# Kernel optimization log

Hardware: AMD Instinct MI355X
Metric: run time of the kernel (lower is better)

## Reference

```python
import jax, jax.numpy as jnp
import numpy as np

L = 8  # uniform FSQ levels per channel (same for every channel)
COMMIT = 0.25


def setup_inputs() -> dict:
    key = jax.random.key(0)
    ks = jax.random.split(key, 8)
    B, S, D, K = 16, 4096, 512, 256
    return {
        "x": jax.random.normal(ks[0], (B, S, D), jnp.float32),
        "codebook": jax.random.normal(ks[1], (K, D), jnp.float32),
        "channel_means": jax.random.normal(ks[2], (D,), jnp.float32) * 0.1,
        "channel_stds": jax.random.uniform(ks[3], (D,), jnp.float32, 0.75, 1.25),
        "w1": jax.random.normal(ks[4], (D, D // 2), jnp.float32) * 0.02,
        "b1": jnp.zeros((D // 2,), jnp.float32),
        "w2": jax.random.normal(ks[5], (D // 2, 2), jnp.float32) * 0.02,
        "b2": jnp.zeros((2,), jnp.float32),
    }


def _uniform_fsq(x):
    # argmin over linspace(-1,1,L) == round to nearest grid point after clamping
    step = 2.0 / (L - 1)
    xc = jnp.clip(x, -1.0, 1.0)
    idx = jnp.round((xc + 1.0) / step)          # [B,S,D] float indices in [0,L-1]
    q = -1.0 + idx * step                        # gathered bound values
    q_st = x + jax.lax.stop_gradient(q - x)
    loss = COMMIT * jnp.mean((x - jax.lax.stop_gradient(q)) ** 2)
    return q_st, idx.astype(jnp.int32), loss


def _kmeans_fsq(x, codebook, means, stds):
    # eval-mode quantize: normalize, cdist+argmin (squared distances share argmin), gather, denorm
    xn = (x - means) / stds                                          # [B,S,D]
    x2 = jnp.sum(xn * xn, axis=-1, keepdims=True)                    # [B,S,1]
    c2 = jnp.sum(codebook * codebook, axis=-1)                       # [K]
    xc = jnp.einsum("bsd,kd->bsk", xn, codebook)                     # [B,S,K]
    d2 = x2 - 2.0 * xc + c2                                          # squared cdist
    indices = jnp.argmin(d2, axis=-1)                                # [B,S]
    q = codebook[indices] * stds + means                             # [B,S,D]
    q_st = x + jax.lax.stop_gradient(q - x)
    loss = COMMIT * jnp.mean((x - jax.lax.stop_gradient(q)) ** 2)
    return q_st, indices, loss


def reference(x, codebook, channel_means, channel_stds, w1, b1, w2, b2):
    # codebook selector on mean-pooled sequence (eval mode: plain softmax)
    pooled = jnp.mean(x, axis=1)                                     # [B,D]
    h = jax.nn.relu(pooled @ w1 + b1)
    logits = h @ w2 + b2                                             # [B,2]
    weights = jax.nn.softmax(logits, axis=-1)                        # [B,2]

    q_u, idx_u, loss_u = _uniform_fsq(x)
    q_k, idx_k, loss_k = _kmeans_fsq(x, codebook, channel_means, channel_stds)

    uw = weights[:, 0][:, None, None]
    kw = weights[:, 1][:, None, None]
    quantized = uw * q_u + kw * q_k                                  # [B,S,D]
    total_loss = loss_u + loss_k
    return quantized, total_loss, idx_k, weights
```

## Files before the change

kernel.cpp:

```cpp
#include <hip/hip_runtime.h>
#include <math.h>

typedef __bf16 bf16x8 __attribute__((ext_vector_type(8)));
typedef float f32x4 __attribute__((ext_vector_type(4)));
typedef unsigned short ushort_t;
typedef unsigned int uint_t;

#define BB 16
#define SS 4096
#define DDIM 512
#define NCODE 256
#define MTOK 65536

#define LOSS_OFF 33554432
#define IDX_OFF  33554433
#define WGT_OFF  33619969

#define WS_LOSS 0
#define WS_LOG  128
#define WS_WGT  192
#define WS_POOL 256
#define WS_C2   8448
#define WS_RSTD 8704
#define WS_BAR  9216

__device__ __forceinline__ void async16(void* lds, const void* gptr) {
  __builtin_amdgcn_global_load_lds(
      (const __attribute__((address_space(1))) unsigned int*)(gptr),
      (__attribute__((address_space(3))) unsigned int*)(lds),
      16, 0, 0);
}

__global__ void init_ws(const float* __restrict__ stds, float* ws) {
  int i = blockIdx.x * blockDim.x + threadIdx.x;
  if (i < 8704) ws[i] = 0.f;
  else if (i < 9216) ws[WS_RSTD + (i - 8704)] = 1.f / stds[i - 8704];
  else if (i == 9216) ws[i] = 0.f;
}

__global__ __launch_bounds__(64) void c2_convert(
    const float* __restrict__ cb, float* __restrict__ c2,
    bf16x8* __restrict__ cbt) {
  const int k = blockIdx.x, t = threadIdx.x;
  const float4* row = (const float4*)(cb + (size_t)k * DDIM);
  float4 a = row[t * 2], b = row[t * 2 + 1];
  float v[8] = {a.x, a.y, a.z, a.w, b.x, b.y, b.z, b.w};
  bf16x8 hi, lo;
  float s = 0.f;
  #pragma unroll
  for (int j = 0; j < 8; j++) {
    s = fmaf(v[j], v[j], s);
    __bf16 hh = (__bf16)v[j];
    hi[j] = hh;
    lo[j] = (__bf16)(v[j] - (float)hh);
  }
  const int kb = t >> 2, q = t & 3;
  const int slot = k * 4 + (q ^ ((k >> 1) & 3));
  cbt[kb * 1024 + slot] = hi;
  cbt[16384 + kb * 1024 + slot] = lo;
  for (int m = 1; m <= 32; m <<= 1) s += __shfl_xor(s, m, 64);
  if (t == 0) c2[k] = s;
}

__global__ __launch_bounds__(512) void pool_kernel(const float* __restrict__ x,
                                                   float* __restrict__ pool) {
  int b = blockIdx.x, sc = blockIdx.y, d = threadIdx.x;
  const float* p = x + ((size_t)b * SS + (size_t)sc * 256) * DDIM + d;
  float s = 0.f;
  #pragma unroll 8
  for (int i = 0; i < 256; i++) s += p[(size_t)i * DDIM];
  atomicAdd(&pool[b * DDIM + d], s);
}

__global__ __launch_bounds__(256) void selector(
    const float* __restrict__ poolsum, const float* __restrict__ w1,
    const float* __restrict__ b1, const float* __restrict__ w2,
    const float* __restrict__ b2, float* __restrict__ wgt,
    float* __restrict__ out) {
  const int b = blockIdx.x, t = threadIdx.x;
  __shared__ float pl[512];
  pl[t] = poolsum[b * DDIM + t] * (1.f / SS);
  pl[t + 256] = poolsum[b * DDIM + 256 + t] * (1.f / SS);
  __syncthreads();
  float acc = 0.f;
  #pragma unroll 8
  for (int d = 0; d < DDIM; d++) acc = fmaf(pl[d], w1[d * 256 + t], acc);
  float hv = fmaxf(acc + b1[t], 0.f);
  float p0 = hv * w2[t * 2], p1 = hv * w2[t * 2 + 1];
  #pragma unroll
  for (int m = 1; m <= 32; m <<= 1) {
    p0 += __shfl_xor(p0, m, 64);
    p1 += __shfl_xor(p1, m, 64);
  }
  __shared__ float r0[4], r1[4];
  const int w = t >> 6;
  if ((t & 63) == 0) { r0[w] = p0; r1[w] = p1; }
  __syncthreads();
  if (t == 0) {
    float l0 = r0[0] + r0[1] + r0[2] + r0[3] + b2[0];
    float l1 = r1[0] + r1[1] + r1[2] + r1[3] + b2[1];
    float mx = fmaxf(l0, l1);
    float e0 = expf(l0 - mx), e1 = expf(l1 - mx);
    float inv = 1.f / (e0 + e1);
    wgt[b * 2] = e0 * inv; wgt[b * 2 + 1] = e1 * inv;
    out[WGT_OFF + b * 2] = e0 * inv; out[WGT_OFF + b * 2 + 1] = e1 * inv;
  }
}

__device__ __forceinline__ void grid_barrier(uint_t* cnt, uint_t nb) {
  __syncthreads();
  if (threadIdx.x == 0) {
    __hip_atomic_fetch_add(cnt, 1u, __ATOMIC_ACQ_REL, __HIP_MEMORY_SCOPE_AGENT);
    while (__hip_atomic_load(cnt, __ATOMIC_ACQUIRE, __HIP_MEMORY_SCOPE_AGENT) < nb)
      __builtin_amdgcn_s_sleep(2);
  }
  __syncthreads();
}

__global__ __launch_bounds__(256, 2) void gemm_fused(
    const float* __restrict__ x, const ushort_t* __restrict__ cbt,
    const float* __restrict__ means, const float* __restrict__ stds,
    const float* __restrict__ rstd, const float* __restrict__ cbf,
    const float* __restrict__ c2g, const float* __restrict__ wsel,
    float* __restrict__ out, float* __restrict__ idxout,
    float* __restrict__ loss_acc, uint_t* __restrict__ bar) {
  __shared__ bf16x8 Ahi[512], Alo[512], Bhi[1024], Blo[1024];
  __shared__ uint_t stash[4][32];
  __shared__ float slu[4], slk[4];
  const int tid = threadIdx.x;
  const int lane = tid & 63, w = tid >> 6;
  const size_t token0 = (size_t)blockIdx.x * 128;
  const int c = lane & 15, quad = lane >> 4;

  f32x4 acc[2][16];
  #pragma unroll
  for (int tt = 0; tt < 2; tt++)
    #pragma unroll
    for (int ct = 0; ct < 16; ct++) {
      f32x4 z = {0.f, 0.f, 0.f, 0.f};
      acc[tt][ct] = z;
    }

  const int r = tid >> 1, h = tid & 1;
  const float* xrow = x + (token0 + r) * DDIM;

  for (int kbi = 0; kbi < 16; kbi++) {
    const int kb = kbi * 32;
    __syncthreads();
    #pragma unroll
    for (int i = 0; i < 4; i++) {
      const int slot = i * 256 + tid;
      async16((void*)&Bhi[slot], (const void*)(cbt + ((size_t)kbi * 1024 + slot) * 8));
      async16((void*)&Blo[slot], (const void*)(cbt + ((size_t)(16384 + kbi * 1024) + slot) * 8));
    }
    #pragma unroll
    for (int sub = 0; sub < 2; sub++) {
      const int q = h * 2 + sub;
      const int kk = kb + q * 8;
      float4 xa = *(const float4*)(xrow + kk);
      float4 xb = *(const float4*)(xrow + kk + 4);
      float4 ma = *(const float4*)(means + kk);
      float4 mb = *(const float4*)(means + kk + 4);
      float4 ra = *(const float4*)(rstd + kk);
      float4 rb = *(const float4*)(rstd + kk + 4);
      float xv[8] = {xa.x, xa.y, xa.z, xa.w, xb.x, xb.y, xb.z, xb.w};
      float mv[8] = {ma.x, ma.y, ma.z, ma.w, mb.x, mb.y, mb.z, mb.w};
      float rv[8] = {ra.x, ra.y, ra.z, ra.w, rb.x, rb.y, rb.z, rb.w};
      bf16x8 hi, lo;
      #pragma unroll
      for (int j = 0; j < 8; j++) {
        float xn = (xv[j] - mv[j]) * rv[j];
        __bf16 hh = (__bf16)xn;
        hi[j] = hh;
        lo[j] = (__bf16)(xn - (float)hh);
      }
      const int p = (q + (r >> 1)) & 3;
      Ahi[r * 4 + p] = hi;
      Alo[r * 4 + p] = lo;
    }
    __syncthreads();

    bf16x8 ahi[2], alo[2];
    #pragma unroll
    for (int tt = 0; tt < 2; tt++) {
      const int rr = w * 32 + tt * 16 + c;
      const int p = (quad + (rr >> 1)) & 3;
      ahi[tt] = Ahi[rr * 4 + p];
      alo[tt] = Alo[rr * 4 + p];
    }
    #pragma unroll
    for (int ct = 0; ct < 16; ct++) {
      const int cf = ct * 16 + c;
      const int slot = cf * 4 + (quad ^ ((cf >> 1) & 3));
      bf16x8 bhi = Bhi[slot];
      bf16x8 blo = Blo[slot];
      #pragma unroll
      for (int tt = 0; tt < 2; tt++) {
        acc[tt][ct] = __builtin_amdgcn_mfma_f32_16x16x32_bf16(ahi[tt], bhi, acc[tt][ct], 0, 0, 0);
        acc[tt][ct] = __builtin_amdgcn_mfma_f32_16x16x32_bf16(ahi[tt], blo, acc[tt][ct], 0, 0, 0);
        acc[tt][ct] = __builtin_amdgcn_mfma_f32_16x16x32_bf16(alo[tt], bhi, acc[tt][ct], 0, 0, 0);
      }
    }
  }

  float c2v[16];
  #pragma unroll
  for (int ct = 0; ct < 16; ct++) c2v[ct] = c2g[ct * 16 + c];

#define LESS(av, ai, bv, bi) ((av) < (bv) || ((av) == (bv) && (ai) < (bi)))
#define INS2(v, i)                                                            \
  if (LESS(v, i, tv1, ti1)) {                                                 \
    tv1 = (v); ti1 = (i);                                                     \
    if (LESS(tv1, ti1, tv0, ti0)) { float tf = tv0; int tj = ti0; tv0 = tv1; ti0 = ti1; tv1 = tf; ti1 = tj; } \
  }

  #pragma unroll
  for (int tt = 0; tt < 2; tt++) {
    #pragma unroll
    for (int reg = 0; reg < 4; reg++) {
      float tv0 = 3.4e38f, tv1 = 3.4e38f;
      int ti0 = 0, ti1 = 0;
      #pragma unroll
      for (int ct = 0; ct < 16; ct++) {
        float vv = fmaf(-2.f, acc[tt][ct][reg], c2v[ct]);
        int ii = ct * 16 + c;
        INS2(vv, ii);
      }
      #pragma unroll
      for (int m = 1; m <= 8; m <<= 1) {
        float ov0 = __shfl_xor(tv0, m, 64), ov1 = __shfl_xor(tv1, m, 64);
        int oi0 = __shfl_xor(ti0, m, 64), oi1 = __shfl_xor(ti1, m, 64);
        INS2(ov0, oi0); INS2(ov1, oi1);
      }
      if (c == 0)
        stash[w][tt * 16 + quad * 4 + reg] = (uint_t)ti0 | ((uint_t)ti1 << 16);
    }
  }
#undef INS2
#undef LESS

  grid_barrier(bar, (uint_t)gridDim.x);

  const int dA = lane * 4;
  const int dB = 256 + lane * 4;
  float4 mA = *(const float4*)(means + dA), mB = *(const float4*)(means + dB);
  float4 sA = *(const float4*)(stds + dA),  sB = *(const float4*)(stds + dB);
  float4 rA = *(const float4*)(rstd + dA),  rB = *(const float4*)(rstd + dB);
  const float step = (float)(2.0 / 7.0);
  const int b = (int)(token0 >> 12);
  const float w0 = wsel[b * 2], w1v = wsel[b * 2 + 1];
  float lu = 0.f, lk = 0.f;

  #pragma unroll 2
  for (int it = 0; it < 32; it++) {
    const size_t token = token0 + (size_t)w * 32 + it;
    const uint_t packed = stash[w][it];
    const int k0 = (int)(packed & 0xffffu), k1 = (int)(packed >> 16);
    const float* xr = x + token * DDIM;
    float4 xA = *(const float4*)(xr + dA);
    float4 xB = *(const float4*)(xr + dB);
    const float* c0 = cbf + (size_t)k0 * DDIM;
    const float* c1 = cbf + (size_t)k1 * DDIM;
    float4 cA0 = *(const float4*)(c0 + dA), cB0 = *(const float4*)(c0 + dB);
    float4 cA1 = *(const float4*)(c1 + dA), cB1 = *(const float4*)(c1 + dB);

    float xnA0 = (xA.x - mA.x) * rA.x, xnA1 = (xA.y - mA.y) * rA.y;
    float xnA2 = (xA.z - mA.z) * rA.z, xnA3 = (xA.w - mA.w) * rA.w;
    float xnB0 = (xB.x - mB.x) * rB.x, xnB1 = (xB.y - mB.y) * rB.y;
    float xnB2 = (xB.z - mB.z) * rB.z, xnB3 = (xB.w - mB.w) * rB.w;

    float d0 = xnA0 * cA0.x + xnA1 * cA0.y + xnA2 * cA0.z + xnA3 * cA0.w +
               xnB0 * cB0.x + xnB1 * cB0.y + xnB2 * cB0.z + xnB3 * cB0.w;
    float d1 = xnA0 * cA1.x + xnA1 * cA1.y + xnA2 * cA1.z + xnA3 * cA1.w +
               xnB0 * cB1.x + xnB1 * cB1.y + xnB2 * cB1.z + xnB3 * cB1.w;
    #pragma unroll
    for (int m = 1; m <= 32; m <<= 1) {
      d0 += __shfl_xor(d0, m, 64);
      d1 += __shfl_xor(d1, m, 64);
    }
    float s0 = fmaf(-2.f, d0, c2g[k0]);
    float s1 = fmaf(-2.f, d1, c2g[k1]);
    const bool take1 = (s1 < s0) || (s1 == s0 && k1 < k0);
    const int bk = take1 ? k1 : k0;
    if (lane == 0) idxout[token] = (float)bk;
    float4 cwA, cwB;
    cwA = take1 ? cA1 : cA0;
    cwB = take1 ? cB1 : cB0;

    float4 oA, oB;
#define DOE(xx, cw, mm, ss, dst)                                              \
    { float xc = fminf(fmaxf(xx, -1.f), 1.f);                                 \
      float fi = rintf(__fdiv_rn(xc + 1.f, step));                            \
      float qq = __fadd_rn(__fmul_rn(fi, step), -1.f);                        \
      float qk = __fadd_rn(__fmul_rn(cw, ss), mm);                            \
      float qu_ = xx + (qq - xx);                                             \
      float qks = xx + (qk - xx);                                             \
      dst = w0 * qu_ + w1v * qks;                                             \
      float du = xx - qq; lu = fmaf(du, du, lu);                              \
      float dk = xx - qk; lk = fmaf(dk, dk, lk); }
    DOE(xA.x, cwA.x, mA.x, sA.x, oA.x)
    DOE(xA.y, cwA.y, mA.y, sA.y, oA.y)
    DOE(xA.z, cwA.z, mA.z, sA.z, oA.z)
    DOE(xA.w, cwA.w, mA.w, sA.w, oA.w)
    DOE(xB.x, cwB.x, mB.x, sB.x, oB.x)
    DOE(xB.y, cwB.y, mB.y, sB.y, oB.y)
    DOE(xB.z, cwB.z, mB.z, sB.z, oB.z)
    DOE(xB.w, cwB.w, mB.w, sB.w, oB.w)
#undef DOE
    f32x4 voA = {oA.x, oA.y, oA.z, oA.w};
    f32x4 voB = {oB.x, oB.y, oB.z, oB.w};
    __builtin_nontemporal_store(voA, (f32x4*)(out + token * DDIM + dA));
    __builtin_nontemporal_store(voB, (f32x4*)(out + token * DDIM + dB));
  }

  for (int m = 1; m <= 32; m <<= 1) {
    lu += __shfl_xor(lu, m, 64);
    lk += __shfl_xor(lk, m, 64);
  }
  if (lane == 0) { slu[w] = lu; slk[w] = lk; }
  __syncthreads();
  if (tid == 0) {
    atomicAdd(loss_acc + 0, slu[0] + slu[1] + slu[2] + slu[3]);
    atomicAdd(loss_acc + 64, slk[0] + slk[1] + slk[2] + slk[3]);
  }
}

__global__ void finalize_kernel(const float* __restrict__ ls, float* __restrict__ out_loss) {
  const float invN = 1.f / ((float)MTOK * (float)DDIM);
  out_loss[0] = 0.25f * (ls[0] * invN) + 0.25f * (ls[64] * invN);
}

extern "C" void kernel_launch(void* const* d_in, const int* in_sizes, int n_in,
                              void* d_out, int out_size, void* d_ws, size_t ws_size,
                              hipStream_t stream) {
  const float* x     = (const float*)d_in[0];
  const float* cbf   = (const float*)d_in[1];
  const float* means = (const float*)d_in[2];
  const float* stds  = (const float*)d_in[3];
  const float* w1    = (const float*)d_in[4];
  const float* b1    = (const float*)d_in[5];
  const float* w2    = (const float*)d_in[6];
  const float* b2    = (const float*)d_in[7];
  float* out = (float*)d_out;
  float* ws  = (float*)d_ws;
  bf16x8* cbt = (bf16x8*)d_out;

  hipLaunchKernelGGL(init_ws, dim3(37), dim3(256), 0, stream, stds, ws);
  hipLaunchKernelGGL(c2_convert, dim3(NCODE), dim3(64), 0, stream, cbf, ws + WS_C2, cbt);
  hipLaunchKernelGGL(pool_kernel, dim3(BB, 16), dim3(512), 0, stream, x, ws + WS_POOL);
  hipLaunchKernelGGL(selector, dim3(BB), dim3(256), 0, stream,
                     ws + WS_POOL, w1, b1, w2, b2, ws + WS_WGT, out);
  hipLaunchKernelGGL(gemm_fused, dim3(MTOK / 128), dim3(256), 0, stream,
                     x, (const ushort_t*)d_out, means, stds, ws + WS_RSTD, cbf,
                     ws + WS_C2, ws + WS_WGT, out, out + IDX_OFF, ws + WS_LOSS,
                     (uint_t*)(ws + WS_BAR));
  hipLaunchKernelGGL(finalize_kernel, dim3(1), dim3(1), 0, stream,
                     ws + WS_LOSS, out + LOSS_OFF);
}
```

Baseline: 386.8 us.

## Fuse mean-pooling and selector MLP into the persistent GEMM kernel

```diff
diff --git a/kernel.cpp b/kernel.cpp
--- a/kernel.cpp
+++ b/kernel.cpp
@@ -23,6 +23,7 @@
 #define WS_C2   8448
 #define WS_RSTD 8704
 #define WS_BAR  9216
+#define WS_BAR2 9217
 
 __device__ __forceinline__ void async16(void* lds, const void* gptr) {
   __builtin_amdgcn_global_load_lds(
@@ -35,7 +36,7 @@
   int i = blockIdx.x * blockDim.x + threadIdx.x;
   if (i < 8704) ws[i] = 0.f;
   else if (i < 9216) ws[WS_RSTD + (i - 8704)] = 1.f / stds[i - 8704];
-  else if (i == 9216) ws[i] = 0.f;
+  else if (i <= 9217) ws[i] = 0.f;
 }
 
 __global__ __launch_bounds__(64) void c2_convert(
@@ -62,51 +63,6 @@
   if (t == 0) c2[k] = s;
 }
 
-__global__ __launch_bounds__(512) void pool_kernel(const float* __restrict__ x,
-                                                   float* __restrict__ pool) {
-  int b = blockIdx.x, sc = blockIdx.y, d = threadIdx.x;
-  const float* p = x + ((size_t)b * SS + (size_t)sc * 256) * DDIM + d;
-  float s = 0.f;
-  #pragma unroll 8
-  for (int i = 0; i < 256; i++) s += p[(size_t)i * DDIM];
-  atomicAdd(&pool[b * DDIM + d], s);
-}
-
-__global__ __launch_bounds__(256) void selector(
-    const float* __restrict__ poolsum, const float* __restrict__ w1,
-    const float* __restrict__ b1, const float* __restrict__ w2,
-    const float* __restrict__ b2, float* __restrict__ wgt,
-    float* __restrict__ out) {
-  const int b = blockIdx.x, t = threadIdx.x;
-  __shared__ float pl[512];
-  pl[t] = poolsum[b * DDIM + t] * (1.f / SS);
-  pl[t + 256] = poolsum[b * DDIM + 256 + t] * (1.f / SS);
-  __syncthreads();
-  float acc = 0.f;
-  #pragma unroll 8
-  for (int d = 0; d < DDIM; d++) acc = fmaf(pl[d], w1[d * 256 + t], acc);
-  float hv = fmaxf(acc + b1[t], 0.f);
-  float p0 = hv * w2[t * 2], p1 = hv * w2[t * 2 + 1];
-  #pragma unroll
-  for (int m = 1; m <= 32; m <<= 1) {
-    p0 += __shfl_xor(p0, m, 64);
-    p1 += __shfl_xor(p1, m, 64);
-  }
-  __shared__ float r0[4], r1[4];
-  const int w = t >> 6;
-  if ((t & 63) == 0) { r0[w] = p0; r1[w] = p1; }
-  __syncthreads();
-  if (t == 0) {
-    float l0 = r0[0] + r0[1] + r0[2] + r0[3] + b2[0];
-    float l1 = r1[0] + r1[1] + r1[2] + r1[3] + b2[1];
-    float mx = fmaxf(l0, l1);
-    float e0 = expf(l0 - mx), e1 = expf(l1 - mx);
-    float inv = 1.f / (e0 + e1);
-    wgt[b * 2] = e0 * inv; wgt[b * 2 + 1] = e1 * inv;
-    out[WGT_OFF + b * 2] = e0 * inv; out[WGT_OFF + b * 2 + 1] = e1 * inv;
-  }
-}
-
 __device__ __forceinline__ void grid_barrier(uint_t* cnt, uint_t nb) {
   __syncthreads();
   if (threadIdx.x == 0) {
@@ -121,15 +77,19 @@
     const float* __restrict__ x, const ushort_t* __restrict__ cbt,
     const float* __restrict__ means, const float* __restrict__ stds,
     const float* __restrict__ rstd, const float* __restrict__ cbf,
-    const float* __restrict__ c2g, const float* __restrict__ wsel,
-    float* __restrict__ out, float* __restrict__ idxout,
-    float* __restrict__ loss_acc, uint_t* __restrict__ bar) {
+    const float* __restrict__ c2g, const float* __restrict__ w1,
+    const float* __restrict__ b1, const float* __restrict__ w2,
+    const float* __restrict__ b2, float* __restrict__ pool,
+    float* __restrict__ wsel, float* __restrict__ out,
+    float* __restrict__ idxout, float* __restrict__ loss_acc,
+    uint_t* __restrict__ bar, uint_t* __restrict__ bar2) {
   __shared__ bf16x8 Ahi[512], Alo[512], Bhi[1024], Blo[1024];
   __shared__ uint_t stash[4][32];
   __shared__ float slu[4], slk[4];
   const int tid = threadIdx.x;
   const int lane = tid & 63, w = tid >> 6;
   const size_t token0 = (size_t)blockIdx.x * 128;
+  const int b = (int)(token0 >> 12);
   const int c = lane & 15, quad = lane >> 4;
 
   f32x4 acc[2][16];
@@ -203,6 +163,25 @@
     }
   }
 
+  {
+    const int ch4 = (tid & 127) * 4;
+    const int rh = tid >> 7;
+    const float* px = x + (token0 + (size_t)rh * 64) * DDIM + ch4;
+    f32x4 p0 = {0.f,0.f,0.f,0.f}, p1 = {0.f,0.f,0.f,0.f};
+    f32x4 p2 = {0.f,0.f,0.f,0.f}, p3 = {0.f,0.f,0.f,0.f};
+    for (int i = 0; i < 64; i += 4) {
+      p0 += *(const f32x4*)(px + (size_t)(i + 0) * DDIM);
+      p1 += *(const f32x4*)(px + (size_t)(i + 1) * DDIM);
+      p2 += *(const f32x4*)(px + (size_t)(i + 2) * DDIM);
+      p3 += *(const f32x4*)(px + (size_t)(i + 3) * DDIM);
+    }
+    f32x4 ps = (p0 + p1) + (p2 + p3);
+    atomicAdd(&pool[b * DDIM + ch4 + 0], ps[0]);
+    atomicAdd(&pool[b * DDIM + ch4 + 1], ps[1]);
+    atomicAdd(&pool[b * DDIM + ch4 + 2], ps[2]);
+    atomicAdd(&pool[b * DDIM + ch4 + 3], ps[3]);
+  }
+
   float c2v[16];
   #pragma unroll
   for (int ct = 0; ct < 16; ct++) c2v[ct] = c2g[ct * 16 + c];
@@ -241,17 +220,57 @@
 
   grid_barrier(bar, (uint_t)gridDim.x);
 
+  __shared__ float selbuf[512];
+  __shared__ float sr0[4], sr1[4];
+  if (blockIdx.x < 16) {
+    const int sb = blockIdx.x;
+    float v0 = __hip_atomic_load(&pool[sb * DDIM + tid], __ATOMIC_RELAXED, __HIP_MEMORY_SCOPE_AGENT);
+    float v1 = __hip_atomic_load(&pool[sb * DDIM + 256 + tid], __ATOMIC_RELAXED, __HIP_MEMORY_SCOPE_AGENT);
+    selbuf[tid] = v0 * (1.f / SS);
+    selbuf[tid + 256] = v1 * (1.f / SS);
+    __syncthreads();
+    float a = 0.f;
+    #pragma unroll 8
+    for (int d = 0; d < DDIM; d++) a = fmaf(selbuf[d], w1[d * 256 + tid], a);
+    float hv = fmaxf(a + b1[tid], 0.f);
+    float q0 = hv * w2[tid * 2], q1 = hv * w2[tid * 2 + 1];
+    #pragma unroll
+    for (int m = 1; m <= 32; m <<= 1) {
+      q0 += __shfl_xor(q0, m, 64);
+      q1 += __shfl_xor(q1, m, 64);
+    }
+    if ((tid & 63) == 0) { sr0[tid >> 6] = q0; sr1[tid >> 6] = q1; }
+    __syncthreads();
+    if (tid == 0) {
+      float l0 = sr0[0] + sr0[1] + sr0[2] + sr0[3] + b2[0];
+      float l1 = sr1[0] + sr1[1] + sr1[2] + sr1[3] + b2[1];
+      float mx = fmaxf(l0, l1);
+      float e0 = expf(l0 - mx), e1 = expf(l1 - mx);
+      float inv = 1.f / (e0 + e1);
+      __hip_atomic_store(&wsel[sb * 2], e0 * inv, __ATOMIC_RELAXED, __HIP_MEMORY_SCOPE_AGENT);
+      __hip_atomic_store(&wsel[sb * 2 + 1], e1 * inv, __ATOMIC_RELAXED, __HIP_MEMORY_SCOPE_AGENT);
+      out[WGT_OFF + sb * 2] = e0 * inv;
+      out[WGT_OFF + sb * 2 + 1] = e1 * inv;
+      __hip_atomic_fetch_add(bar2, 1u, __ATOMIC_RELEASE, __HIP_MEMORY_SCOPE_AGENT);
+    }
+  }
+  if (tid == 0) {
+    while (__hip_atomic_load(bar2, __ATOMIC_ACQUIRE, __HIP_MEMORY_SCOPE_AGENT) < 16u)
+      __builtin_amdgcn_s_sleep(2);
+  }
+  __syncthreads();
+
   const int dA = lane * 4;
   const int dB = 256 + lane * 4;
   float4 mA = *(const float4*)(means + dA), mB = *(const float4*)(means + dB);
   float4 sA = *(const float4*)(stds + dA),  sB = *(const float4*)(stds + dB);
   float4 rA = *(const float4*)(rstd + dA),  rB = *(const float4*)(rstd + dB);
   const float step = (float)(2.0 / 7.0);
-  const int b = (int)(token0 >> 12);
-  const float w0 = wsel[b * 2], w1v = wsel[b * 2 + 1];
+  const float w0 = __hip_atomic_load(&wsel[b * 2], __ATOMIC_RELAXED, __HIP_MEMORY_SCOPE_AGENT);
+  const float w1v = __hip_atomic_load(&wsel[b * 2 + 1], __ATOMIC_RELAXED, __HIP_MEMORY_SCOPE_AGENT);
   float lu = 0.f, lk = 0.f;
 
-  #pragma unroll 2
+  #pragma unroll 4
   for (int it = 0; it < 32; it++) {
     const size_t token = token0 + (size_t)w * 32 + it;
     const uint_t packed = stash[w][it];
@@ -345,15 +364,13 @@
   float* ws  = (float*)d_ws;
   bf16x8* cbt = (bf16x8*)d_out;
 
-  hipLaunchKernelGGL(init_ws, dim3(37), dim3(256), 0, stream, stds, ws);
+  hipLaunchKernelGGL(init_ws, dim3(38), dim3(256), 0, stream, stds, ws);
   hipLaunchKernelGGL(c2_convert, dim3(NCODE), dim3(64), 0, stream, cbf, ws + WS_C2, cbt);
-  hipLaunchKernelGGL(pool_kernel, dim3(BB, 16), dim3(512), 0, stream, x, ws + WS_POOL);
-  hipLaunchKernelGGL(selector, dim3(BB), dim3(256), 0, stream,
-                     ws + WS_POOL, w1, b1, w2, b2, ws + WS_WGT, out);
   hipLaunchKernelGGL(gemm_fused, dim3(MTOK / 128), dim3(256), 0, stream,
                      x, (const ushort_t*)d_out, means, stds, ws + WS_RSTD, cbf,
-                     ws + WS_C2, ws + WS_WGT, out, out + IDX_OFF, ws + WS_LOSS,
-                     (uint_t*)(ws + WS_BAR));
+                     ws + WS_C2, w1, b1, w2, b2, ws + WS_POOL, ws + WS_WGT,
+                     out, out + IDX_OFF, ws + WS_LOSS,
+                     (uint_t*)(ws + WS_BAR), (uint_t*)(ws + WS_BAR2));
   hipLaunchKernelGGL(finalize_kernel, dim3(1), dim3(1), 0, stream,
                      ws + WS_LOSS, out + LOSS_OFF);
 }
```

Result: slower. 485.7 us (+25.6%).
